# Kernel tuning notes

Hardware: AMD Instinct MI355X
Metric: run time of the kernel (lower is better)

The kernel has to match this reference:

```python
import jax, jax.numpy as jnp
import numpy as np

KS = 6            # kernel_size, (KS-2)%4 == 0
LEVELS = 4
PAD = (KS - 2) // 4  # = 1


def antireflect_pad(x, p):
    # odd (antisymmetric) reflection about the boundary samples
    left = 2.0 * x[:, :, :1] - jnp.flip(x[:, :, 1:p + 1], axis=-1)
    right = 2.0 * x[:, :, -1:] - jnp.flip(x[:, :, -p - 1:-1], axis=-1)
    return jnp.concatenate([left, x, right], axis=-1)


def make_polyphase(f):
    # torch: flip(f.reshape(-1,2).permute(1,0), dims=(1,)).unsqueeze(1) -> (2,1,KS//2)
    return jnp.flip(f.reshape(-1, 2).T, axis=1)[:, None, :]


def conv1d(x, k):
    # x: (c,1,L), k: (2,1,KS//2); cross-correlation, VALID, matches F.conv1d
    return jax.lax.conv_general_dilated(x, k, window_strides=(1,), padding='VALID',
                                        dimension_numbers=('NCH', 'OIH', 'NCH'))


def synth_branch(x, k):
    # pad -> tiny conv -> sub-pixel upsample (interleave the 2 polyphase channels)
    c = x.shape[0]
    y = conv1d(antireflect_pad(x, PAD), k)      # (c, 2, L)
    return y.transpose(0, 2, 1).reshape(c, 1, -1)  # (c, 1, 2L)


def setup_inputs() -> dict:
    key = jax.random.key(0)
    ks = jax.random.split(key, 7)
    c, L = 64, 16384
    return {
        'signal': jax.random.normal(ks[0], (c, 1, L), dtype=jnp.float32),
        'd0': jax.random.normal(ks[1], (c, 1, L * 8), dtype=jnp.float32),
        'd1': jax.random.normal(ks[2], (c, 1, L * 4), dtype=jnp.float32),
        'd2': jax.random.normal(ks[3], (c, 1, L * 2), dtype=jnp.float32),
        'd3': jax.random.normal(ks[4], (c, 1, L), dtype=jnp.float32),
        'h': jax.random.normal(ks[5], (KS,), dtype=jnp.float32),
        'g': jax.random.normal(ks[6], (KS,), dtype=jnp.float32),
    }


def reference(signal, d0, d1, d2, d3, h, g):
    hk = make_polyphase(h)
    gk = make_polyphase(g)
    details = [d0, d1, d2, d3]
    for i in range(LEVELS - 1, -1, -1):
        signal = synth_branch(signal, hk) + synth_branch(details[i], gk)
    return signal
```

## Files before the change

kernel.cpp:

```cpp
#include <hip/hip_runtime.h>

#define C_CH   64
#define L0     16384
#define B_OUT  4096
#define NCHUNK ((L0 * 16) / B_OUT)

typedef float f32x4 __attribute__((ext_vector_type(4)));
typedef float f32x2 __attribute__((ext_vector_type(2)));

struct Taps {
    float he0, he1, he2, ho0, ho1, ho2;
    float ge0, ge1, ge2, go0, go1, go2;
};

template <bool GLOBAL_OUT>
__device__ __forceinline__ void synth_level(
    const float* __restrict__ xp, int xlo, int Lx,
    const float* __restrict__ dp,
    float* __restrict__ yp, int ylo, int yhi,
    const Taps& T, int tid, int nthr)
{
    const int tlo = ylo >> 1, thi = yhi >> 1;
    const int tA = (tlo == 0) ? 1 : tlo;
    const int tB = (thi == Lx - 1) ? (thi - 1) : thi;

    int tV0 = (tA < 2) ? 2 : tA;
    tV0 = (tV0 + 1) & ~1;
    int tVmax = tB - 1; if (tVmax > Lx - 4) tVmax = Lx - 4;
    const int nvec = (tVmax >= tV0) ? (((tVmax - tV0) >> 1) + 1) : 0;

    for (int i = tid; i < nvec; i += nthr) {
        const int t0 = tV0 + 2 * i;
        const f32x2 b01 = *reinterpret_cast<const f32x2*>(dp + t0 - 2);
        const f32x2 b23 = *reinterpret_cast<const f32x2*>(dp + t0);
        const f32x2 b45 = *reinterpret_cast<const f32x2*>(dp + t0 + 2);
        const float d0 = b01.y, d1 = b23.x, d2 = b23.y, d3 = b45.x;
        const float a0 = xp[t0 - 1 - xlo];
        const float a1 = xp[t0     - xlo];
        const float a2 = xp[t0 + 1 - xlo];
        const float a3 = xp[t0 + 2 - xlo];
        f32x4 v;
        v.x = a0*T.he0 + a1*T.he1 + a2*T.he2 + d0*T.ge0 + d1*T.ge1 + d2*T.ge2;
        v.y = a0*T.ho0 + a1*T.ho1 + a2*T.ho2 + d0*T.go0 + d1*T.go1 + d2*T.go2;
        v.z = a1*T.he0 + a2*T.he1 + a3*T.he2 + d1*T.ge0 + d2*T.ge1 + d3*T.ge2;
        v.w = a1*T.ho0 + a2*T.ho1 + a3*T.ho2 + d1*T.go0 + d2*T.go1 + d3*T.go2;
        f32x4* dst = reinterpret_cast<f32x4*>(yp + (2 * t0 - ylo));
        if (GLOBAL_OUT) __builtin_nontemporal_store(v, dst);
        else            *dst = v;
    }

    const int tE0 = tV0 + 2 * nvec;
    for (int t = tA + tid; t < tV0; t += nthr) {
        const float a0 = xp[t-1-xlo], a1 = xp[t-xlo], a2 = xp[t+1-xlo];
        const float d0 = dp[t-1], d1 = dp[t], d2 = dp[t+1];
        const float ve = a0*T.he0 + a1*T.he1 + a2*T.he2 + d0*T.ge0 + d1*T.ge1 + d2*T.ge2;
        const float vo = a0*T.ho0 + a1*T.ho1 + a2*T.ho2 + d0*T.go0 + d1*T.go1 + d2*T.go2;
        *reinterpret_cast<f32x2*>(yp + (2*t - ylo)) = f32x2{ve, vo};
    }
    for (int t = tE0 + tid; t <= tB; t += nthr) {
        const float a0 = xp[t-1-xlo], a1 = xp[t-xlo], a2 = xp[t+1-xlo];
        const float d0 = dp[t-1], d1 = dp[t], d2 = dp[t+1];
        const float ve = a0*T.he0 + a1*T.he1 + a2*T.he2 + d0*T.ge0 + d1*T.ge1 + d2*T.ge2;
        const float vo = a0*T.ho0 + a1*T.ho1 + a2*T.ho2 + d0*T.go0 + d1*T.go1 + d2*T.go2;
        *reinterpret_cast<f32x2*>(yp + (2*t - ylo)) = f32x2{ve, vo};
    }
    if (tid == 0) {
        if (tlo == 0) {
            const float x0 = xp[0 - xlo], x1 = xp[1 - xlo];
            const float dd0 = dp[0], dd1 = dp[1];
            const float a0 = 2.0f*x0 - x1, b0 = 2.0f*dd0 - dd1;
            const float ve = a0*T.he0 + x0*T.he1 + x1*T.he2 + b0*T.ge0 + dd0*T.ge1 + dd1*T.ge2;
            const float vo = a0*T.ho0 + x0*T.ho1 + x1*T.ho2 + b0*T.go0 + dd0*T.go1 + dd1*T.go2;
            *reinterpret_cast<f32x2*>(yp + (0 - ylo)) = f32x2{ve, vo};
        }
        if (thi == Lx - 1) {
            const int t = Lx - 1;
            const float xm = xp[t-1-xlo], xl = xp[t-xlo];
            const float dm = dp[t-1], dl = dp[t];
            const float a2 = 2.0f*xl - xm, b2 = 2.0f*dl - dm;
            const float ve = xm*T.he0 + xl*T.he1 + a2*T.he2 + dm*T.ge0 + dl*T.ge1 + b2*T.ge2;
            const float vo = xm*T.ho0 + xl*T.ho1 + a2*T.ho2 + dm*T.go0 + dl*T.go1 + b2*T.go2;
            *reinterpret_cast<f32x2*>(yp + (2*t - ylo)) = f32x2{ve, vo};
        }
    }
}

__global__ __launch_bounds__(256) void iwt_fused_kernel(
    const float* __restrict__ sig,
    const float* __restrict__ d0,
    const float* __restrict__ d1,
    const float* __restrict__ d2,
    const float* __restrict__ d3,
    const float* __restrict__ h,
    const float* __restrict__ g,
    float* __restrict__ out)
{
    const int c     = blockIdx.y;
    const int chunk = blockIdx.x;
    const int tid   = threadIdx.x;
    const int nthr  = blockDim.x;

    Taps T;
    T.he0 = h[4]; T.he1 = h[2]; T.he2 = h[0];
    T.ho0 = h[5]; T.ho1 = h[3]; T.ho2 = h[1];
    T.ge0 = g[4]; T.ge1 = g[2]; T.ge2 = g[0];
    T.go0 = g[5]; T.go1 = g[3]; T.go2 = g[1];

    __shared__ __align__(16) float s1[520];
    __shared__ __align__(16) float s2[1032];
    __shared__ __align__(16) float s3[2056];

    const int L1 = 2*L0, L2 = 4*L0, L3 = 8*L0, L4 = 16*L0;

    const int lo4 = chunk * B_OUT;
    const int hi4 = lo4 + B_OUT - 1;
    int lo3 = (lo4 >> 1) - 4; if (lo3 < 0) lo3 = 0;
    int hi3 = (hi4 >> 1) + 1; if (hi3 > L3 - 1) hi3 = L3 - 1;
    int lo2 = (lo3 >> 1) - 2; if (lo2 < 0) lo2 = 0;
    int hi2 = (hi3 >> 1) + 1; if (hi2 > L2 - 1) hi2 = L2 - 1;
    int lo1 = (lo2 >> 1) - 2; if (lo1 < 0) lo1 = 0;
    int hi1 = (hi2 >> 1) + 1; if (hi1 > L1 - 1) hi1 = L1 - 1;

    const float* s0p = sig + (size_t)c * L0;
    const float* d3p = d3  + (size_t)c * L0;
    const float* d2p = d2  + (size_t)c * L1;
    const float* d1p = d1  + (size_t)c * L2;
    const float* d0p = d0  + (size_t)c * L3;
    float*       outp = out + (size_t)c * L4;

    synth_level<false>(s0p, 0, L0, d3p, s1, lo1, hi1, T, tid, nthr);
    __syncthreads();
    synth_level<false>(s1, lo1, L1, d2p, s2, lo2, hi2, T, tid, nthr);
    __syncthreads();
    synth_level<false>(s2, lo2, L2, d1p, s3, lo3, hi3, T, tid, nthr);
    __syncthreads();
    synth_level<true >(s3, lo3, L3, d0p, outp + lo4, lo4, hi4, T, tid, nthr);
}

extern "C" void kernel_launch(void* const* d_in, const int* in_sizes, int n_in,
                              void* d_out, int out_size, void* d_ws, size_t ws_size,
                              hipStream_t stream) {
    const float* sig = (const float*)d_in[0];
    const float* d0  = (const float*)d_in[1];
    const float* d1  = (const float*)d_in[2];
    const float* d2  = (const float*)d_in[3];
    const float* d3  = (const float*)d_in[4];
    const float* h   = (const float*)d_in[5];
    const float* g   = (const float*)d_in[6];
    float* out = (float*)d_out;

    dim3 grid(NCHUNK, C_CH);
    iwt_fused_kernel<<<grid, 256, 0, stream>>>(sig, d0, d1, d2, d3, h, g, out);
}
```

Measured before the change: 28.74 us.

## Split interior chunks into per-wavefront independent tiles without block barriers

Interior chunks now give each 64-lane wavefront its own 1024-sample output tile, with halo recomputation in private shared-memory slices. This removes the three __syncthreads between levels, and all global loads for every level are issued up front so their latency overlaps. Edge chunks keep the old block-wide path, which is now scalar-only because the vectorized path in synth_level was removed. The cost is redundant halo work per wave and higher register pressure from the prefetched data.

```diff
diff --git a/kernel.cpp b/kernel.cpp
--- a/kernel.cpp
+++ b/kernel.cpp
@@ -24,49 +24,16 @@
     const int tA = (tlo == 0) ? 1 : tlo;
     const int tB = (thi == Lx - 1) ? (thi - 1) : thi;
 
-    int tV0 = (tA < 2) ? 2 : tA;
-    tV0 = (tV0 + 1) & ~1;
-    int tVmax = tB - 1; if (tVmax > Lx - 4) tVmax = Lx - 4;
-    const int nvec = (tVmax >= tV0) ? (((tVmax - tV0) >> 1) + 1) : 0;
-
-    for (int i = tid; i < nvec; i += nthr) {
-        const int t0 = tV0 + 2 * i;
-        const f32x2 b01 = *reinterpret_cast<const f32x2*>(dp + t0 - 2);
-        const f32x2 b23 = *reinterpret_cast<const f32x2*>(dp + t0);
-        const f32x2 b45 = *reinterpret_cast<const f32x2*>(dp + t0 + 2);
-        const float d0 = b01.y, d1 = b23.x, d2 = b23.y, d3 = b45.x;
-        const float a0 = xp[t0 - 1 - xlo];
-        const float a1 = xp[t0     - xlo];
-        const float a2 = xp[t0 + 1 - xlo];
-        const float a3 = xp[t0 + 2 - xlo];
-        f32x4 v;
-        v.x = a0*T.he0 + a1*T.he1 + a2*T.he2 + d0*T.ge0 + d1*T.ge1 + d2*T.ge2;
-        v.y = a0*T.ho0 + a1*T.ho1 + a2*T.ho2 + d0*T.go0 + d1*T.go1 + d2*T.go2;
-        v.z = a1*T.he0 + a2*T.he1 + a3*T.he2 + d1*T.ge0 + d2*T.ge1 + d3*T.ge2;
-        v.w = a1*T.ho0 + a2*T.ho1 + a3*T.ho2 + d1*T.go0 + d2*T.go1 + d3*T.go2;
-        f32x4* dst = reinterpret_cast<f32x4*>(yp + (2 * t0 - ylo));
-        if (GLOBAL_OUT) __builtin_nontemporal_store(v, dst);
-        else            *dst = v;
-    }
-
-    const int tE0 = tV0 + 2 * nvec;
-    for (int t = tA + tid; t < tV0; t += nthr) {
+    for (int t = tA + tid; t <= tB; t += nthr) {
         const float a0 = xp[t-1-xlo], a1 = xp[t-xlo], a2 = xp[t+1-xlo];
         const float d0 = dp[t-1], d1 = dp[t], d2 = dp[t+1];
         const float ve = a0*T.he0 + a1*T.he1 + a2*T.he2 + d0*T.ge0 + d1*T.ge1 + d2*T.ge2;
         const float vo = a0*T.ho0 + a1*T.ho1 + a2*T.ho2 + d0*T.go0 + d1*T.go1 + d2*T.go2;
         *reinterpret_cast<f32x2*>(yp + (2*t - ylo)) = f32x2{ve, vo};
     }
-    for (int t = tE0 + tid; t <= tB; t += nthr) {
-        const float a0 = xp[t-1-xlo], a1 = xp[t-xlo], a2 = xp[t+1-xlo];
-        const float d0 = dp[t-1], d1 = dp[t], d2 = dp[t+1];
-        const float ve = a0*T.he0 + a1*T.he1 + a2*T.he2 + d0*T.ge0 + d1*T.ge1 + d2*T.ge2;
-        const float vo = a0*T.ho0 + a1*T.ho1 + a2*T.ho2 + d0*T.go0 + d1*T.go1 + d2*T.go2;
-        *reinterpret_cast<f32x2*>(yp + (2*t - ylo)) = f32x2{ve, vo};
-    }
     if (tid == 0) {
         if (tlo == 0) {
-            const float x0 = xp[0 - xlo], x1 = xp[1 - xlo];
+            const float x0 = xp[0-xlo], x1 = xp[1-xlo];
             const float dd0 = dp[0], dd1 = dp[1];
             const float a0 = 2.0f*x0 - x1, b0 = 2.0f*dd0 - dd1;
             const float ve = a0*T.he0 + x0*T.he1 + x1*T.he2 + b0*T.ge0 + dd0*T.ge1 + dd1*T.ge2;
@@ -86,19 +53,14 @@
 }
 
 __global__ __launch_bounds__(256) void iwt_fused_kernel(
-    const float* __restrict__ sig,
-    const float* __restrict__ d0,
-    const float* __restrict__ d1,
-    const float* __restrict__ d2,
-    const float* __restrict__ d3,
-    const float* __restrict__ h,
-    const float* __restrict__ g,
-    float* __restrict__ out)
+    const float* __restrict__ sig, const float* __restrict__ d0,
+    const float* __restrict__ d1,  const float* __restrict__ d2,
+    const float* __restrict__ d3,  const float* __restrict__ h,
+    const float* __restrict__ g,   float* __restrict__ out)
 {
     const int c     = blockIdx.y;
     const int chunk = blockIdx.x;
     const int tid   = threadIdx.x;
-    const int nthr  = blockDim.x;
 
     Taps T;
     T.he0 = h[4]; T.he1 = h[2]; T.he2 = h[0];
@@ -106,20 +68,11 @@
     T.ge0 = g[4]; T.ge1 = g[2]; T.ge2 = g[0];
     T.go0 = g[5]; T.go1 = g[3]; T.go2 = g[1];
 
-    __shared__ __align__(16) float s1[520];
-    __shared__ __align__(16) float s2[1032];
-    __shared__ __align__(16) float s3[2056];
+    __shared__ __align__(16) float s1[544];
+    __shared__ __align__(16) float s2[1056];
+    __shared__ __align__(16) float s3[2080];
 
     const int L1 = 2*L0, L2 = 4*L0, L3 = 8*L0, L4 = 16*L0;
-
-    const int lo4 = chunk * B_OUT;
-    const int hi4 = lo4 + B_OUT - 1;
-    int lo3 = (lo4 >> 1) - 4; if (lo3 < 0) lo3 = 0;
-    int hi3 = (hi4 >> 1) + 1; if (hi3 > L3 - 1) hi3 = L3 - 1;
-    int lo2 = (lo3 >> 1) - 2; if (lo2 < 0) lo2 = 0;
-    int hi2 = (hi3 >> 1) + 1; if (hi2 > L2 - 1) hi2 = L2 - 1;
-    int lo1 = (lo2 >> 1) - 2; if (lo1 < 0) lo1 = 0;
-    int hi1 = (hi2 >> 1) + 1; if (hi1 > L1 - 1) hi1 = L1 - 1;
 
     const float* s0p = sig + (size_t)c * L0;
     const float* d3p = d3  + (size_t)c * L0;
@@ -128,13 +81,109 @@
     const float* d0p = d0  + (size_t)c * L3;
     float*       outp = out + (size_t)c * L4;
 
-    synth_level<false>(s0p, 0, L0, d3p, s1, lo1, hi1, T, tid, nthr);
-    __syncthreads();
-    synth_level<false>(s1, lo1, L1, d2p, s2, lo2, hi2, T, tid, nthr);
-    __syncthreads();
-    synth_level<false>(s2, lo2, L2, d1p, s3, lo3, hi3, T, tid, nthr);
-    __syncthreads();
-    synth_level<true >(s3, lo3, L3, d0p, outp + lo4, lo4, hi4, T, tid, nthr);
+    if (chunk == 0 || chunk == NCHUNK - 1) {
+        const int lo4 = chunk * B_OUT;
+        const int hi4 = lo4 + B_OUT - 1;
+        int lo3 = (lo4 >> 1) - 4; if (lo3 < 0) lo3 = 0;
+        int hi3 = (hi4 >> 1) + 1; if (hi3 > L3 - 1) hi3 = L3 - 1;
+        int lo2 = (lo3 >> 1) - 2; if (lo2 < 0) lo2 = 0;
+        int hi2 = (hi3 >> 1) + 1; if (hi2 > L2 - 1) hi2 = L2 - 1;
+        int lo1 = (lo2 >> 1) - 2; if (lo1 < 0) lo1 = 0;
+        int hi1 = (hi2 >> 1) + 1; if (hi1 > L1 - 1) hi1 = L1 - 1;
+
+        synth_level<false>(s0p, 0, L0, d3p, s1, lo1, hi1, T, tid, 256);
+        __syncthreads();
+        synth_level<false>(s1, lo1, L1, d2p, s2, lo2, hi2, T, tid, 256);
+        __syncthreads();
+        synth_level<false>(s2, lo2, L2, d1p, s3, lo3, hi3, T, tid, 256);
+        __syncthreads();
+        synth_level<true >(s3, lo3, L3, d0p, outp + lo4, lo4, hi4, T, tid, 256);
+        return;
+    }
+
+    const int w = tid >> 6, l = tid & 63;
+    float* __restrict__ s1w = s1 + w * 136;
+    float* __restrict__ s2w = s2 + w * 264;
+    float* __restrict__ s3w = s3 + w * 520;
+
+    const int T4 = ((chunk * B_OUT) >> 1) + (w << 9);
+    const int T3 = T4 >> 1, T2 = T3 >> 1, T1 = T2 >> 1;
+    const int ml = (l < 3) ? l : 0;
+
+    const int t1i[2] = { T1 - 2 + l, T1 + 62 + ml };
+    float xs[2][3], e3[2][3];
+#pragma unroll
+    for (int i = 0; i < 2; ++i) {
+        const int t = t1i[i];
+        xs[i][0] = s0p[t-1]; xs[i][1] = s0p[t]; xs[i][2] = s0p[t+1];
+        e3[i][0] = d3p[t-1]; e3[i][1] = d3p[t]; e3[i][2] = d3p[t+1];
+    }
+    const int t2i[3] = { T2 - 2 + l, T2 + 62 + l, T2 + 126 + ml };
+    float e2[3][3];
+#pragma unroll
+    for (int i = 0; i < 3; ++i) {
+        const int t = t2i[i];
+        e2[i][0] = d2p[t-1]; e2[i][1] = d2p[t]; e2[i][2] = d2p[t+1];
+    }
+    const int t3i[5] = { T3 - 2 + l, T3 + 62 + l, T3 + 126 + l, T3 + 190 + l,
+                         T3 + 254 + ml };
+    float e1[5][3];
+#pragma unroll
+    for (int i = 0; i < 5; ++i) {
+        const int t = t3i[i];
+        e1[i][0] = d1p[t-1]; e1[i][1] = d1p[t]; e1[i][2] = d1p[t+1];
+    }
+    f32x2 e0[4][3];
+#pragma unroll
+    for (int i = 0; i < 4; ++i) {
+        const int t0 = T4 + 2*(l + (i << 6));
+        e0[i][0] = *reinterpret_cast<const f32x2*>(d0p + t0 - 2);
+        e0[i][1] = *reinterpret_cast<const f32x2*>(d0p + t0);
+        e0[i][2] = *reinterpret_cast<const f32x2*>(d0p + t0 + 2);
+    }
+
+#pragma unroll
+    for (int i = 0; i < 2; ++i) {
+        const float a0 = xs[i][0], a1 = xs[i][1], a2 = xs[i][2];
+        const float b0 = e3[i][0], b1 = e3[i][1], b2 = e3[i][2];
+        const float ve = a0*T.he0 + a1*T.he1 + a2*T.he2 + b0*T.ge0 + b1*T.ge1 + b2*T.ge2;
+        const float vo = a0*T.ho0 + a1*T.ho1 + a2*T.ho2 + b0*T.go0 + b1*T.go1 + b2*T.go2;
+        if (i == 0 || l < 3)
+            *reinterpret_cast<f32x2*>(s1w + (2*t1i[i] - (T2-4))) = f32x2{ve, vo};
+    }
+#pragma unroll
+    for (int i = 0; i < 3; ++i) {
+        const int o = t2i[i] - (T2 - 4);
+        const float a0 = s1w[o-1], a1 = s1w[o], a2 = s1w[o+1];
+        const float b0 = e2[i][0], b1 = e2[i][1], b2 = e2[i][2];
+        const float ve = a0*T.he0 + a1*T.he1 + a2*T.he2 + b0*T.ge0 + b1*T.ge1 + b2*T.ge2;
+        const float vo = a0*T.ho0 + a1*T.ho1 + a2*T.ho2 + b0*T.go0 + b1*T.go1 + b2*T.go2;
+        if (i < 2 || l < 3)
+            *reinterpret_cast<f32x2*>(s2w + (2*t2i[i] - (T3-4))) = f32x2{ve, vo};
+    }
+#pragma unroll
+    for (int i = 0; i < 5; ++i) {
+        const int o = t3i[i] - (T3 - 4);
+        const float a0 = s2w[o-1], a1 = s2w[o], a2 = s2w[o+1];
+        const float b0 = e1[i][0], b1 = e1[i][1], b2 = e1[i][2];
+        const float ve = a0*T.he0 + a1*T.he1 + a2*T.he2 + b0*T.ge0 + b1*T.ge1 + b2*T.ge2;
+        const float vo = a0*T.ho0 + a1*T.ho1 + a2*T.ho2 + b0*T.go0 + b1*T.go1 + b2*T.go2;
+        if (i < 4 || l < 3)
+            *reinterpret_cast<f32x2*>(s3w + (2*t3i[i] - (T4-4))) = f32x2{ve, vo};
+    }
+#pragma unroll
+    for (int i = 0; i < 4; ++i) {
+        const int t0 = T4 + 2*(l + (i << 6));
+        const int o  = t0 - (T4 - 4);
+        const float a0 = s3w[o-1], a1 = s3w[o], a2 = s3w[o+1], a3 = s3w[o+2];
+        const float b0 = e0[i][0].y, b1 = e0[i][1].x, b2 = e0[i][1].y, b3 = e0[i][2].x;
+        f32x4 v;
+        v.x = a0*T.he0 + a1*T.he1 + a2*T.he2 + b0*T.ge0 + b1*T.ge1 + b2*T.ge2;
+        v.y = a0*T.ho0 + a1*T.ho1 + a2*T.ho2 + b0*T.go0 + b1*T.go1 + b2*T.go2;
+        v.z = a1*T.he0 + a2*T.he1 + a3*T.he2 + b1*T.ge0 + b2*T.ge1 + b3*T.ge2;
+        v.w = a1*T.ho0 + a2*T.ho1 + a3*T.ho2 + b1*T.go0 + b2*T.go1 + b3*T.go2;
+        __builtin_nontemporal_store(v, reinterpret_cast<f32x4*>(outp + 2*t0));
+    }
 }
 
 extern "C" void kernel_launch(void* const* d_in, const int* in_sizes, int n_in,
```

New measurement: 31.09 us. 1.08x slower.

## Compose four synthesis levels into one direct polyphase filter per output

Applied to the files above, without the earlier changes.

Precomputes the composed multi-level filter coefficients in shared memory and computes each output sample directly from the signal and all four detail arrays, eliminating the per-level shared-memory intermediates and barriers. Boundary regions are handled by a dedicated extra block per channel using the old per-level path. This removes the recomputation of halos and sync overhead, but switches to scalar stores and gathers with more global loads per output, and uses fewer blocks.

```diff
diff --git a/kernel.cpp b/kernel.cpp
--- a/kernel.cpp
+++ b/kernel.cpp
@@ -1,11 +1,8 @@
 #include <hip/hip_runtime.h>
 
-#define C_CH   64
-#define L0     16384
-#define B_OUT  4096
-#define NCHUNK ((L0 * 16) / B_OUT)
+#define C_CH 64
+#define L0   16384
 
-typedef float f32x4 __attribute__((ext_vector_type(4)));
 typedef float f32x2 __attribute__((ext_vector_type(2)));
 
 struct Taps {
@@ -24,40 +21,7 @@
     const int tA = (tlo == 0) ? 1 : tlo;
     const int tB = (thi == Lx - 1) ? (thi - 1) : thi;
 
-    int tV0 = (tA < 2) ? 2 : tA;
-    tV0 = (tV0 + 1) & ~1;
-    int tVmax = tB - 1; if (tVmax > Lx - 4) tVmax = Lx - 4;
-    const int nvec = (tVmax >= tV0) ? (((tVmax - tV0) >> 1) + 1) : 0;
-
-    for (int i = tid; i < nvec; i += nthr) {
-        const int t0 = tV0 + 2 * i;
-        const f32x2 b01 = *reinterpret_cast<const f32x2*>(dp + t0 - 2);
-        const f32x2 b23 = *reinterpret_cast<const f32x2*>(dp + t0);
-        const f32x2 b45 = *reinterpret_cast<const f32x2*>(dp + t0 + 2);
-        const float d0 = b01.y, d1 = b23.x, d2 = b23.y, d3 = b45.x;
-        const float a0 = xp[t0 - 1 - xlo];
-        const float a1 = xp[t0     - xlo];
-        const float a2 = xp[t0 + 1 - xlo];
-        const float a3 = xp[t0 + 2 - xlo];
-        f32x4 v;
-        v.x = a0*T.he0 + a1*T.he1 + a2*T.he2 + d0*T.ge0 + d1*T.ge1 + d2*T.ge2;
-        v.y = a0*T.ho0 + a1*T.ho1 + a2*T.ho2 + d0*T.go0 + d1*T.go1 + d2*T.go2;
-        v.z = a1*T.he0 + a2*T.he1 + a3*T.he2 + d1*T.ge0 + d2*T.ge1 + d3*T.ge2;
-        v.w = a1*T.ho0 + a2*T.ho1 + a3*T.ho2 + d1*T.go0 + d2*T.go1 + d3*T.go2;
-        f32x4* dst = reinterpret_cast<f32x4*>(yp + (2 * t0 - ylo));
-        if (GLOBAL_OUT) __builtin_nontemporal_store(v, dst);
-        else            *dst = v;
-    }
-
-    const int tE0 = tV0 + 2 * nvec;
-    for (int t = tA + tid; t < tV0; t += nthr) {
-        const float a0 = xp[t-1-xlo], a1 = xp[t-xlo], a2 = xp[t+1-xlo];
-        const float d0 = dp[t-1], d1 = dp[t], d2 = dp[t+1];
-        const float ve = a0*T.he0 + a1*T.he1 + a2*T.he2 + d0*T.ge0 + d1*T.ge1 + d2*T.ge2;
-        const float vo = a0*T.ho0 + a1*T.ho1 + a2*T.ho2 + d0*T.go0 + d1*T.go1 + d2*T.go2;
-        *reinterpret_cast<f32x2*>(yp + (2*t - ylo)) = f32x2{ve, vo};
-    }
-    for (int t = tE0 + tid; t <= tB; t += nthr) {
+    for (int t = tA + tid; t <= tB; t += nthr) {
         const float a0 = xp[t-1-xlo], a1 = xp[t-xlo], a2 = xp[t+1-xlo];
         const float d0 = dp[t-1], d1 = dp[t], d2 = dp[t+1];
         const float ve = a0*T.he0 + a1*T.he1 + a2*T.he2 + d0*T.ge0 + d1*T.ge1 + d2*T.ge2;
@@ -66,7 +30,7 @@
     }
     if (tid == 0) {
         if (tlo == 0) {
-            const float x0 = xp[0 - xlo], x1 = xp[1 - xlo];
+            const float x0 = xp[0-xlo], x1 = xp[1-xlo];
             const float dd0 = dp[0], dd1 = dp[1];
             const float a0 = 2.0f*x0 - x1, b0 = 2.0f*dd0 - dd1;
             const float ve = a0*T.he0 + x0*T.he1 + x1*T.he2 + b0*T.ge0 + dd0*T.ge1 + dd1*T.ge2;
@@ -85,41 +49,20 @@
     }
 }
 
-__global__ __launch_bounds__(256) void iwt_fused_kernel(
-    const float* __restrict__ sig,
-    const float* __restrict__ d0,
-    const float* __restrict__ d1,
-    const float* __restrict__ d2,
-    const float* __restrict__ d3,
-    const float* __restrict__ h,
-    const float* __restrict__ g,
-    float* __restrict__ out)
+__global__ __launch_bounds__(256) void iwt_composed_kernel(
+    const float* __restrict__ sig, const float* __restrict__ d0,
+    const float* __restrict__ d1,  const float* __restrict__ d2,
+    const float* __restrict__ d3,  const float* __restrict__ h,
+    const float* __restrict__ g,   float* __restrict__ out)
 {
-    const int c     = blockIdx.y;
-    const int chunk = blockIdx.x;
-    const int tid   = threadIdx.x;
-    const int nthr  = blockDim.x;
-
-    Taps T;
-    T.he0 = h[4]; T.he1 = h[2]; T.he2 = h[0];
-    T.ho0 = h[5]; T.ho1 = h[3]; T.ho2 = h[1];
-    T.ge0 = g[4]; T.ge1 = g[2]; T.ge2 = g[0];
-    T.go0 = g[5]; T.go1 = g[3]; T.go2 = g[1];
-
-    __shared__ __align__(16) float s1[520];
-    __shared__ __align__(16) float s2[1032];
-    __shared__ __align__(16) float s3[2056];
+    const int c   = blockIdx.y;
+    const int tid = threadIdx.x;
 
     const int L1 = 2*L0, L2 = 4*L0, L3 = 8*L0, L4 = 16*L0;
 
-    const int lo4 = chunk * B_OUT;
-    const int hi4 = lo4 + B_OUT - 1;
-    int lo3 = (lo4 >> 1) - 4; if (lo3 < 0) lo3 = 0;
-    int hi3 = (hi4 >> 1) + 1; if (hi3 > L3 - 1) hi3 = L3 - 1;
-    int lo2 = (lo3 >> 1) - 2; if (lo2 < 0) lo2 = 0;
-    int hi2 = (hi3 >> 1) + 1; if (hi2 > L2 - 1) hi2 = L2 - 1;
-    int lo1 = (lo2 >> 1) - 2; if (lo1 < 0) lo1 = 0;
-    int hi1 = (hi2 >> 1) + 1; if (hi1 > L1 - 1) hi1 = L1 - 1;
+    __shared__ float cbuf[224];
+    __shared__ float w2h[16], w2g[16], w3h[36], w3g[36];
+    __shared__ __align__(16) float s1b[48], s2b[48], s3b[48];
 
     const float* s0p = sig + (size_t)c * L0;
     const float* d3p = d3  + (size_t)c * L0;
@@ -128,13 +71,113 @@
     const float* d0p = d0  + (size_t)c * L3;
     float*       outp = out + (size_t)c * L4;
 
-    synth_level<false>(s0p, 0, L0, d3p, s1, lo1, hi1, T, tid, nthr);
+    if (blockIdx.x == 32) {
+        Taps T;
+        T.he0 = h[4]; T.he1 = h[2]; T.he2 = h[0];
+        T.ho0 = h[5]; T.ho1 = h[3]; T.ho2 = h[1];
+        T.ge0 = g[4]; T.ge1 = g[2]; T.ge2 = g[0];
+        T.go0 = g[5]; T.go1 = g[3]; T.go2 = g[1];
+
+        synth_level<false>(s0p, 0, L0, d3p, s1b, 0, 9,  T, tid, 256);
+        __syncthreads();
+        synth_level<false>(s1b, 0, L1, d2p, s2b, 0, 17, T, tid, 256);
+        __syncthreads();
+        synth_level<false>(s2b, 0, L2, d1p, s3b, 0, 32, T, tid, 256);
+        __syncthreads();
+        synth_level<true >(s3b, 0, L3, d0p, outp, 0, 63, T, tid, 256);
+        __syncthreads();
+        synth_level<false>(s0p, 0,     L0, d3p, s1b, L1-12, L1-1, T, tid, 256);
+        __syncthreads();
+        synth_level<false>(s1b, L1-12, L1, d2p, s2b, L2-20, L2-1, T, tid, 256);
+        __syncthreads();
+        synth_level<false>(s2b, L2-20, L2, d1p, s3b, L3-36, L3-1, T, tid, 256);
+        __syncthreads();
+        synth_level<true >(s3b, L3-36, L3, d0p, outp + (L4-64), L4-64, L4-1, T, tid, 256);
+        return;
+    }
+
+    for (int i = tid; i < 224; i += 256) cbuf[i] = 0.0f;
+    if (tid < 32) {
+        const float* f = (tid < 16) ? h : g;
+        const int v = (tid & 15) - 6;
+        float acc = 0.0f;
+        for (int u = -2; u <= 3; ++u) {
+            const int x = v - 2*u;
+            if (x >= -2 && x <= 3) acc += f[u+2] * h[x+2];
+        }
+        if (tid < 16) w2h[v+6] = acc; else w2g[v+6] = acc;
+    }
     __syncthreads();
-    synth_level<false>(s1, lo1, L1, d2p, s2, lo2, hi2, T, tid, nthr);
+    if (tid < 72) {
+        const bool hs = (tid < 36);
+        const int v = (hs ? tid : tid - 36) - 14;
+        const float* W2 = hs ? w2h : w2g;
+        float acc = 0.0f;
+        for (int u = -6; u <= 9; ++u) {
+            const int x = v - 2*u;
+            if (x >= -2 && x <= 3) acc += W2[u+6] * h[x+2];
+        }
+        if (hs) w3h[v+14] = acc; else w3g[v+14] = acc;
+    }
     __syncthreads();
-    synth_level<false>(s2, lo2, L2, d1p, s3, lo3, hi3, T, tid, nthr);
+    if (tid < 152) {
+        const bool hs = (tid < 76);
+        const int v = (hs ? tid : tid - 76) - 30;
+        const float* W3 = hs ? w3h : w3g;
+        float acc = 0.0f;
+        for (int u = -14; u <= 21; ++u) {
+            const int x = v - 2*u;
+            if (x >= -2 && x <= 3) acc += W3[u+14] * h[x+2];
+        }
+        cbuf[(hs ? 0 : 80) + v + 32] = acc;
+    }
+    if (tid >= 192 && tid < 228) cbuf[164 + (tid - 192)] = w3g[tid - 192];
+    if (tid >= 228 && tid < 244) cbuf[200 + (tid - 228)] = w2g[tid - 228];
+    if (tid >= 244 && tid < 250) cbuf[216 + (tid - 244)] = g[tid - 244];
     __syncthreads();
-    synth_level<true >(s3, lo3, L3, d0p, outp + lo4, lo4, hi4, T, tid, nthr);
+
+    const int l  = tid & 63, wv = tid >> 6;
+    const int rr = l & 15,  j  = l >> 4;
+    const int m0 = (rr - 2)  >> 1;
+    const int m1 = (rr - 6)  >> 2;
+    const int m2 = (rr - 14) >> 3;
+
+    float cS[5], cT[5], cU[5], cV[4], cW[3];
+#pragma unroll
+    for (int k = 0; k < 5; ++k) {
+        cS[k] = cbuf[      rr - 16*k + 64];
+        cT[k] = cbuf[ 80 + rr - 16*k + 64];
+        cU[k] = cbuf[160 + rr - 8*(m2+k) + 18];
+    }
+#pragma unroll
+    for (int k = 0; k < 4; ++k)
+        cV[k] = cbuf[200 + rr - 4*(m1+k) + 6];
+#pragma unroll
+    for (int i = 0; i < 3; ++i)
+        cW[i] = cbuf[216 + rr - 2*(m0+i) + 2];
+
+    const int Wc = blockIdx.x * 4 + wv;
+    for (int it = 0; it < 32; ++it) {
+        const int rho = Wc * 32 + it;
+        if (rho >= 4094) break;
+        const int nb = 64 + (rho << 6);
+        const int q  = (nb >> 4) + j;
+
+        const float* sq = s0p + q;
+        const float* tq = d3p + q;
+        const float* uq = d2p + 2*q + m2;
+        const float* vq = d1p + 4*q + m1;
+        const float* wq = d0p + 8*q + m0;
+
+        float acc;
+        acc  = sq[-2]*cS[0] + sq[-1]*cS[1] + sq[0]*cS[2] + sq[1]*cS[3] + sq[2]*cS[4];
+        acc += tq[-2]*cT[0] + tq[-1]*cT[1] + tq[0]*cT[2] + tq[1]*cT[3] + tq[2]*cT[4];
+        acc += uq[0]*cU[0] + uq[1]*cU[1] + uq[2]*cU[2] + uq[3]*cU[3] + uq[4]*cU[4];
+        acc += vq[0]*cV[0] + vq[1]*cV[1] + vq[2]*cV[2] + vq[3]*cV[3];
+        acc += wq[0]*cW[0] + wq[1]*cW[1] + wq[2]*cW[2];
+
+        __builtin_nontemporal_store(acc, outp + nb + (j << 4) + rr);
+    }
 }
 
 extern "C" void kernel_launch(void* const* d_in, const int* in_sizes, int n_in,
@@ -149,6 +192,6 @@
     const float* g   = (const float*)d_in[6];
     float* out = (float*)d_out;
 
-    dim3 grid(NCHUNK, C_CH);
-    iwt_fused_kernel<<<grid, 256, 0, stream>>>(sig, d0, d1, d2, d3, h, g, out);
+    dim3 grid(33, C_CH);
+    iwt_composed_kernel<<<grid, 256, 0, stream>>>(sig, d0, d1, d2, d3, h, g, out);
 }
```

Measured after the change: 67.01 us. +133.1%, slower.
